# Performance work log

Hardware: AMD Instinct MI355X
Metric: run time of the kernel (lower is better)

## Reference

```python
import jax, jax.numpy as jnp
import numpy as np
from jax import lax

EPS = 1e-5
CLIP = 1.3  # Hardtanh(-1.3, 1.3)


def hardtanh(v):
    return jnp.clip(v, -CLIP, CLIP)


def binarize(v):
    # sign() forward with straight-through (identity) gradient, as in BCNN BinarizeF
    return v + lax.stop_gradient(jnp.sign(v) - v)


def bc_conv(x, w):
    # binarized conv: binarize both activations and weights, 3x3, stride 1, pad 1
    return lax.conv_general_dilated(
        binarize(x), binarize(w),
        window_strides=(1, 1), padding=((1, 1), (1, 1)),
        dimension_numbers=("NCHW", "OIHW", "NCHW"))


def batchnorm(v, gamma, beta):
    # batch statistics over (N, H, W), per-channel affine (DC_Bn4 variant)
    mean = jnp.mean(v, axis=(0, 2, 3), keepdims=True)
    var = jnp.var(v, axis=(0, 2, 3), keepdims=True)
    inv = lax.rsqrt(var + EPS)
    return (v - mean) * inv * gamma[None, :, None, None] + beta[None, :, None, None]


def setup_inputs() -> dict:
    key = jax.random.key(0)
    k_x, k_w1, k_w2 = jax.random.split(key, 3)
    C = 32
    x = jax.random.normal(k_x, (16, C, 224, 224), dtype=jnp.float32)
    w1 = jax.random.normal(k_w1, (C, C, 3, 3), dtype=jnp.float32) * 0.1
    w2 = jax.random.normal(k_w2, (C, C, 3, 3), dtype=jnp.float32) * 0.1
    g1 = jnp.ones((C,), jnp.float32); b1 = jnp.zeros((C,), jnp.float32)
    g2 = jnp.ones((C,), jnp.float32); b2 = jnp.zeros((C,), jnp.float32)
    return {"x": x, "w1": w1, "g1": g1, "b1": b1, "w2": w2, "g2": g2, "b2": b2}


def reference(x, w1, g1, b1, w2, g2, b2):
    y = batchnorm(bc_conv(hardtanh(x), w1), g1, b1)
    y = batchnorm(bc_conv(hardtanh(y), w2), g2, b2)
    return x + y
```

## Files before the change

kernel.cpp:

```cpp
#include <hip/hip_runtime.h>
#include <stdint.h>

#define NB 16
#define CC 32
#define HH 224
#define WW 224
#define HWP (HH*WW)
#define NHWP (NB*HWP)
#define PW 226
#define PSZ (PW*PW)

#define OFF_S1   0u
#define OFF_S2   3268864u
#define OFF_WP1  6537728u
#define OFF_WP2  6538880u
#define OFF_SQ1  6540032u
#define OFF_SQ2  6540288u
#define OFF_SUM1 6540544u
#define OFF_SUM2 6540672u

__global__ void __launch_bounds__(256) k_setup(const uint32_t* __restrict__ w1,
                                               const uint32_t* __restrict__ w2,
                                               char* __restrict__ ws) {
    int t = blockIdx.x * 256 + threadIdx.x;
    if (t < 576) {
        const uint32_t* w = (t < 288) ? w1 : w2;
        uint32_t* o = (uint32_t*)(ws + ((t < 288) ? OFF_WP1 : OFF_WP2));
        int idx = (t < 288) ? t : t - 288;
        int oc = idx / 9, k = idx - oc * 9;
        uint32_t word = 0;
        for (int i = 0; i < 32; ++i)
            word |= (w[(oc * 32 + i) * 9 + k] >> 31) << i;
        o[idx] = word;
    } else if (t < 768) {
        ((uint32_t*)(ws + OFF_SQ1))[t - 576] = 0u;
    } else if (t >= 1024 && t < 1024 + 28800) {
        int b = t - 1024;
        uint32_t* buf = (uint32_t*)(ws + ((b < 14400) ? OFF_S1 : OFF_S2));
        int bb = (b < 14400) ? b : b - 14400;
        int n = bb / 900;
        int e = bb - n * 900;
        int row, col;
        if (e < 226)      { row = 0;   col = e; }
        else if (e < 452) { row = 225; col = e - 226; }
        else { int k = e - 452; row = 1 + (k >> 1); col = (k & 1) ? 225 : 0; }
        buf[(size_t)n * PSZ + row * PW + col] = 0u;
    }
}

__global__ void __launch_bounds__(256) k_packx(const uint32_t* __restrict__ x,
                                               uint32_t* __restrict__ sp) {
    int t = blockIdx.x * 256 + threadIdx.x;
    int n = t / (HWP / 4);
    int rem4 = t - n * (HWP / 4);
    int px0 = rem4 * 4;
    int r = px0 / WW;
    int cw0 = px0 - r * WW;
    const uint32_t* xp = x + (size_t)n * CC * HWP + px0;
    uint32_t w0 = 0, w1 = 0, w2 = 0, w3 = 0;
    #pragma unroll
    for (int c = 0; c < 32; ++c) {
        uint4 v = *reinterpret_cast<const uint4*>(xp + (size_t)c * HWP);
        w0 |= (v.x >> 31) << c;
        w1 |= (v.y >> 31) << c;
        w2 |= (v.z >> 31) << c;
        w3 |= (v.w >> 31) << c;
    }
    uint32_t* op = sp + (size_t)n * PSZ + (r + 1) * PW + (cw0 + 1);
    op[0] = w0; op[1] = w1; op[2] = w2; op[3] = w3;
}

__device__ __forceinline__ void stage_lds(const uint32_t* __restrict__ wp,
                                          uint32_t (*Wl)[12], int (*Ctab)[32]) {
    for (int i = threadIdx.x; i < 288; i += 256) {
        int oc = i / 9, k = i - oc * 9;
        Wl[oc][k] = wp[i];
    }
    for (int i = threadIdx.x; i < 512; i += 256) {
        int ty = i >> 5, oc = i & 31;
        int s = 0;
        #pragma unroll
        for (int t = 0; t < 9; ++t) {
            int dh = t / 3 - 1, dw = t % 3 - 1;
            bool pad = ((ty & 1) && dh < 0) || ((ty & 2) && dh > 0) ||
                       ((ty & 4) && dw < 0) || ((ty & 8) && dw > 0);
            if (pad) s += 32 - 2 * __popc(wp[oc * 9 + t]);
        }
        Ctab[ty][oc] = s;
    }
}

__device__ __forceinline__ void decode_grp(int t, int& n, int& r, int& cw0) {
    n = t / 12544;
    int rem = t - n * 12544;
    r = rem / 56;
    cw0 = (rem - r * 56) * 4;
}

#define LOAD_TAPS18(base)                                                        \
    uint32_t u0 = (base)[-PW-1], u1 = (base)[-PW],   u2 = (base)[-PW+1],         \
             u3 = (base)[-PW+2], u4 = (base)[-PW+3], u5 = (base)[-PW+4];         \
    uint32_t m0 = (base)[-1],    m1 = (base)[0],     m2 = (base)[1],             \
             m3 = (base)[2],     m4 = (base)[3],     m5 = (base)[4];             \
    uint32_t l0 = (base)[PW-1],  l1 = (base)[PW],    l2 = (base)[PW+1],          \
             l3 = (base)[PW+2],  l4 = (base)[PW+3],  l5 = (base)[PW+4];

#define CONV4L(oc_)                                                              \
    int ocl = (oc_);                                                             \
    asm volatile("" : "+v"(ocl));                                                \
    const uint32_t* wr = &Wl[ocl][0];                                            \
    uint32_t w0 = wr[0], w1 = wr[1], w2 = wr[2], w3 = wr[3], w4 = wr[4],         \
             w5 = wr[5], w6 = wr[6], w7 = wr[7], w8 = wr[8];                     \
    int pc0 = __popc(u0^w0)+__popc(u1^w1)+__popc(u2^w2)                          \
            + __popc(m0^w3)+__popc(m1^w4)+__popc(m2^w5)                          \
            + __popc(l0^w6)+__popc(l1^w7)+__popc(l2^w8);                         \
    int pc1 = __popc(u1^w0)+__popc(u2^w1)+__popc(u3^w2)                          \
            + __popc(m1^w3)+__popc(m2^w4)+__popc(m3^w5)                          \
            + __popc(l1^w6)+__popc(l2^w7)+__popc(l3^w8);                         \
    int pc2 = __popc(u2^w0)+__popc(u3^w1)+__popc(u4^w2)                          \
            + __popc(m2^w3)+__popc(m3^w4)+__popc(m4^w5)                          \
            + __popc(l2^w6)+__popc(l3^w7)+__popc(l4^w8);                         \
    int pc3 = __popc(u3^w0)+__popc(u4^w1)+__popc(u5^w2)                          \
            + __popc(m3^w3)+__popc(m4^w4)+__popc(m5^w5)                          \
            + __popc(l3^w6)+__popc(l4^w7)+__popc(l5^w8);                         \
    int c0 = 288 - 2*pc0 - Ctab[ty0][ocl];                                       \
    int c1 = 288 - 2*pc1 - Ctab[rb][ocl];                                        \
    int c2 = 288 - 2*pc2 - Ctab[rb][ocl];                                        \
    int c3 = 288 - 2*pc3 - Ctab[ty3][ocl];

#define DECODE_BORDER()                                                          \
    int rb = (r == 0) ? 1 : (r == HH - 1) ? 2 : 0;                               \
    int ty0 = rb | ((cw0 == 0) ? 4 : 0);                                         \
    int ty3 = rb | ((cw0 == WW - 4) ? 8 : 0);

__global__ void __launch_bounds__(256) k_stats(const uint32_t* __restrict__ sp,
                                               const uint32_t* __restrict__ wp,
                                               int* __restrict__ g_sum,
                                               unsigned long long* __restrict__ g_sq) {
    __shared__ __align__(16) uint32_t Wl[32][12];
    __shared__ int Ctab[16][32];
    stage_lds(wp, Wl, Ctab);
    __syncthreads();

    int t = blockIdx.x * 256 + threadIdx.x;
    int n, r, cw0; decode_grp(t, n, r, cw0);
    const uint32_t* base = sp + (size_t)n * PSZ + (r + 1) * PW + (cw0 + 1);
    LOAD_TAPS18(base)
    DECODE_BORDER()

    int lane = threadIdx.x & 63;
    int lane31 = lane & 31;
    int myS = 0, myQ = 0;
    #pragma unroll
    for (int oc = 0; oc < 32; ++oc) {
        CONV4L(oc)
        int s = c0 + c1 + c2 + c3;
        int q = c0*c0 + c1*c1 + c2*c2 + c3*c3;
        #pragma unroll
        for (int d = 1; d <= 16; d <<= 1) {
            s += __shfl_xor(s, d, 64);
            q += __shfl_xor(q, d, 64);
        }
        if (lane31 == oc) { myS = s; myQ = q; }
    }
    myS += __shfl_xor(myS, 32, 64);
    myQ += __shfl_xor(myQ, 32, 64);

    __shared__ int ls[4][32], lq[4][32];
    int wid = threadIdx.x >> 6;
    if (lane < 32) { ls[wid][lane] = myS; lq[wid][lane] = myQ; }
    __syncthreads();
    if (threadIdx.x < 32) {
        int s = ls[0][threadIdx.x] + ls[1][threadIdx.x] + ls[2][threadIdx.x] + ls[3][threadIdx.x];
        int q = lq[0][threadIdx.x] + lq[1][threadIdx.x] + lq[2][threadIdx.x] + lq[3][threadIdx.x];
        atomicAdd(&g_sum[threadIdx.x], s);
        atomicAdd(&g_sq[threadIdx.x], (unsigned long long)(long long)q);
    }
}

__device__ __forceinline__ void build_affine(const int* __restrict__ g_sum,
                                             const unsigned long long* __restrict__ g_sq,
                                             const float* __restrict__ gamma,
                                             const float* __restrict__ beta,
                                             float* aL, float* dL) {
    if (threadIdx.x < 32) {
        int c = threadIdx.x;
        double M = (double)NHWP;
        double mean = (double)g_sum[c] / M;
        double ex2 = (double)(long long)g_sq[c] / M;
        double var = ex2 - mean * mean;
        double inv = 1.0 / sqrt(var + 1e-5);
        double aa = inv * (double)gamma[c];
        aL[c] = (float)aa;
        dL[c] = (float)((double)beta[c] - aa * mean);
    }
}

__global__ void __launch_bounds__(256) k_sign(const uint32_t* __restrict__ sp,
                                              const uint32_t* __restrict__ wp,
                                              const int* __restrict__ g_sum,
                                              const unsigned long long* __restrict__ g_sq,
                                              const float* __restrict__ gamma,
                                              const float* __restrict__ beta,
                                              uint32_t* __restrict__ op) {
    __shared__ __align__(16) uint32_t Wl[32][12];
    __shared__ int Ctab[16][32];
    __shared__ float aL[32], dL[32];
    stage_lds(wp, Wl, Ctab);
    build_affine(g_sum, g_sq, gamma, beta, aL, dL);
    __syncthreads();

    int t = blockIdx.x * 256 + threadIdx.x;
    int n, r, cw0; decode_grp(t, n, r, cw0);
    const uint32_t* base = sp + (size_t)n * PSZ + (r + 1) * PW + (cw0 + 1);
    LOAD_TAPS18(base)
    DECODE_BORDER()

    uint32_t wd0 = 0, wd1 = 0, wd2 = 0, wd3 = 0;
    #pragma unroll
    for (int oc = 0; oc < 32; ++oc) {
        CONV4L(oc)
        float a = aL[ocl], d = dL[ocl];
        wd0 |= (__float_as_uint(fmaf(a, (float)c0, d)) >> 31) << oc;
        wd1 |= (__float_as_uint(fmaf(a, (float)c1, d)) >> 31) << oc;
        wd2 |= (__float_as_uint(fmaf(a, (float)c2, d)) >> 31) << oc;
        wd3 |= (__float_as_uint(fmaf(a, (float)c3, d)) >> 31) << oc;
    }
    uint32_t* o = op + (size_t)n * PSZ + (r + 1) * PW + (cw0 + 1);
    o[0] = wd0; o[1] = wd1; o[2] = wd2; o[3] = wd3;
}

__global__ void __launch_bounds__(256) k_res(const uint32_t* __restrict__ sp,
                                             const uint32_t* __restrict__ wp,
                                             const int* __restrict__ g_sum,
                                             const unsigned long long* __restrict__ g_sq,
                                             const float* __restrict__ gamma,
                                             const float* __restrict__ beta,
                                             const float* __restrict__ x,
                                             float* __restrict__ out) {
    __shared__ __align__(16) uint32_t Wl[32][12];
    __shared__ int Ctab[16][32];
    __shared__ float aL[32], dL[32];
    stage_lds(wp, Wl, Ctab);
    build_affine(g_sum, g_sq, gamma, beta, aL, dL);
    __syncthreads();

    int t = blockIdx.x * 256 + threadIdx.x;
    int n, r, cw0; decode_grp(t, n, r, cw0);
    const uint32_t* base = sp + (size_t)n * PSZ + (r + 1) * PW + (cw0 + 1);
    LOAD_TAPS18(base)
    DECODE_BORDER()

    size_t pix = (size_t)n * CC * HWP + (size_t)r * WW + cw0;
    #pragma unroll
    for (int oc = 0; oc < 32; ++oc) {
        CONV4L(oc)
        float a = aL[ocl], d = dL[ocl];
        float4 xv = *reinterpret_cast<const float4*>(x + pix + (size_t)ocl * HWP);
        float4 ov;
        ov.x = xv.x + fmaf(a, (float)c0, d);
        ov.y = xv.y + fmaf(a, (float)c1, d);
        ov.z = xv.z + fmaf(a, (float)c2, d);
        ov.w = xv.w + fmaf(a, (float)c3, d);
        *reinterpret_cast<float4*>(out + pix + (size_t)ocl * HWP) = ov;
    }
}

extern "C" void kernel_launch(void* const* d_in, const int* in_sizes, int n_in,
                              void* d_out, int out_size, void* d_ws, size_t ws_size,
                              hipStream_t stream) {
    const float* x  = (const float*)d_in[0];
    const float* w1 = (const float*)d_in[1];
    const float* g1 = (const float*)d_in[2];
    const float* b1 = (const float*)d_in[3];
    const float* w2 = (const float*)d_in[4];
    const float* g2 = (const float*)d_in[5];
    const float* b2 = (const float*)d_in[6];
    float* out = (float*)d_out;

    char* ws = (char*)d_ws;
    uint32_t* s1  = (uint32_t*)(ws + OFF_S1);
    uint32_t* s2  = (uint32_t*)(ws + OFF_S2);
    uint32_t* wp1 = (uint32_t*)(ws + OFF_WP1);
    uint32_t* wp2 = (uint32_t*)(ws + OFF_WP2);
    unsigned long long* sq1 = (unsigned long long*)(ws + OFF_SQ1);
    unsigned long long* sq2 = (unsigned long long*)(ws + OFF_SQ2);
    int* sum1 = (int*)(ws + OFF_SUM1);
    int* sum2 = (int*)(ws + OFF_SUM2);

    k_setup<<<120, 256, 0, stream>>>((const uint32_t*)w1, (const uint32_t*)w2, ws);
    k_packx<<<784, 256, 0, stream>>>((const uint32_t*)x, s1);
    k_stats<<<784, 256, 0, stream>>>(s1, wp1, sum1, sq1);
    k_sign <<<784, 256, 0, stream>>>(s1, wp1, sum1, sq1, g1, b1, s2);
    k_stats<<<784, 256, 0, stream>>>(s2, wp2, sum2, sq2);
    k_res  <<<784, 256, 0, stream>>>(s2, wp2, sum2, sq2, g2, b2, x, out);
}
```

Before: 318.2 us.

## Replace XNOR-popcount binary conv with int8 MFMA in stats and sign kernels

```diff
diff --git a/kernel.cpp b/kernel.cpp
--- a/kernel.cpp
+++ b/kernel.cpp
@@ -15,9 +15,12 @@
 #define OFF_WP1  6537728u
 #define OFF_WP2  6538880u
 #define OFF_SQ1  6540032u
-#define OFF_SQ2  6540288u
-#define OFF_SUM1 6540544u
-#define OFF_SUM2 6540672u
+#define OFF_SQ2  6544128u
+#define OFF_SUM1 6548224u
+#define OFF_SUM2 6550272u
+
+typedef int v4i    __attribute__((ext_vector_type(4)));
+typedef int i32x16 __attribute__((ext_vector_type(16)));
 
 __global__ void __launch_bounds__(256) k_setup(const uint32_t* __restrict__ w1,
                                                const uint32_t* __restrict__ w2,
@@ -32,10 +35,10 @@
         for (int i = 0; i < 32; ++i)
             word |= (w[(oc * 32 + i) * 9 + k] >> 31) << i;
         o[idx] = word;
-    } else if (t < 768) {
+    } else if (t < 3648) {
         ((uint32_t*)(ws + OFF_SQ1))[t - 576] = 0u;
-    } else if (t >= 1024 && t < 1024 + 28800) {
-        int b = t - 1024;
+    } else if (t >= 4096 && t < 4096 + 28800) {
+        int b = t - 4096;
         uint32_t* buf = (uint32_t*)(ws + ((b < 14400) ? OFF_S1 : OFF_S2));
         int bb = (b < 14400) ? b : b - 14400;
         int n = bb / 900;
@@ -68,6 +71,143 @@
     }
     uint32_t* op = sp + (size_t)n * PSZ + (r + 1) * PW + (cw0 + 1);
     op[0] = w0; op[1] = w1; op[2] = w2; op[3] = w3;
+}
+
+#define ASTRIDE 48
+#define AROW (226*ASTRIDE)
+
+__device__ __forceinline__ uint32_t spread4(uint32_t nib) {
+    uint32_t s = (nib & 1u) | ((nib & 2u) << 7) | ((nib & 4u) << 14) | ((nib & 8u) << 21);
+    return 0x01010101u ^ (s * 0xFEu);
+}
+
+__device__ __forceinline__ i32x16 conv_mfma(const uint32_t* __restrict__ sp,
+                                            const uint32_t* __restrict__ wp,
+                                            int n, int r, char* At) {
+    for (int s = threadIdx.x; s < 3 * 226; s += 448) {
+        int dr = s / 226, cc = s - dr * 226;
+        int srow = r - 1 + dr, scol = cc - 1;
+        uint32_t d8[8];
+        if (srow < 0 || srow >= HH || scol < 0 || scol >= WW) {
+            #pragma unroll
+            for (int i = 0; i < 8; ++i) d8[i] = 0u;
+        } else {
+            uint32_t w = sp[(size_t)n * PSZ + (srow + 1) * PW + (scol + 1)];
+            #pragma unroll
+            for (int i = 0; i < 8; ++i) d8[i] = spread4((w >> (4 * i)) & 0xFu);
+        }
+        uint32_t* p = (uint32_t*)(At + s * ASTRIDE);
+        *(uint4*)(p)     = make_uint4(d8[0], d8[1], d8[2], d8[3]);
+        *(uint4*)(p + 4) = make_uint4(d8[4], d8[5], d8[6], d8[7]);
+    }
+
+    int l = threadIdx.x & 63;
+    int oc = l & 31, kb = (l >> 5) * 16;
+    v4i bf[9];
+    #pragma unroll
+    for (int t = 0; t < 9; ++t) {
+        uint32_t w = wp[oc * 9 + t];
+        uint32_t r0 = spread4((w >> (kb))      & 0xFu);
+        uint32_t r1 = spread4((w >> (kb + 4))  & 0xFu);
+        uint32_t r2 = spread4((w >> (kb + 8))  & 0xFu);
+        uint32_t r3 = spread4((w >> (kb + 12)) & 0xFu);
+        bf[t] = v4i{(int)r0, (int)r1, (int)r2, (int)r3};
+    }
+    __syncthreads();
+
+    int wavebase = (threadIdx.x >> 6) * 32;
+    int base = (wavebase + (l & 31)) * ASTRIDE + (l >> 5) * 16;
+
+    i32x16 acc = {0,0,0,0,0,0,0,0,0,0,0,0,0,0,0,0};
+    #pragma unroll
+    for (int dh = 0; dh < 3; ++dh) {
+        #pragma unroll
+        for (int dw = 0; dw < 3; ++dw) {
+            v4i a = *reinterpret_cast<const v4i*>(At + base + dh * AROW + dw * ASTRIDE);
+            acc = __builtin_amdgcn_mfma_i32_32x32x32_i8(a, bf[dh * 3 + dw], acc, 0, 0, 0);
+        }
+    }
+    return acc;
+}
+
+__global__ void __launch_bounds__(448) k_stats(const uint32_t* __restrict__ sp,
+                                               const uint32_t* __restrict__ wp,
+                                               int* __restrict__ g_sum,
+                                               unsigned long long* __restrict__ g_sq) {
+    __shared__ __align__(16) char At[3 * 226 * ASTRIDE];
+    __shared__ int ls[7][32], lq[7][32];
+
+    int n = blockIdx.x / HH, r = blockIdx.x - n * HH;
+    i32x16 acc = conv_mfma(sp, wp, n, r, At);
+
+    int l = threadIdx.x & 63;
+    int s = 0, q = 0;
+    #pragma unroll
+    for (int g = 0; g < 16; ++g) { int c = acc[g]; s += c; q += c * c; }
+    s += __shfl_xor(s, 32, 64);
+    q += __shfl_xor(q, 32, 64);
+    int wid = threadIdx.x >> 6;
+    if (l < 32) { ls[wid][l] = s; lq[wid][l] = q; }
+    __syncthreads();
+    if (threadIdx.x < 32) {
+        int S = 0, Q = 0;
+        #pragma unroll
+        for (int w = 0; w < 7; ++w) { S += ls[w][threadIdx.x]; Q += lq[w][threadIdx.x]; }
+        int bin = blockIdx.x & 15;
+        atomicAdd(&g_sum[bin * 32 + threadIdx.x], S);
+        atomicAdd(&g_sq[bin * 32 + threadIdx.x], (unsigned long long)(long long)Q);
+    }
+}
+
+__device__ __forceinline__ void build_affine16(const int* __restrict__ g_sum,
+                                               const unsigned long long* __restrict__ g_sq,
+                                               const float* __restrict__ gamma,
+                                               const float* __restrict__ beta,
+                                               float* aL, float* dL) {
+    if (threadIdx.x < 32) {
+        int c = threadIdx.x;
+        int Si = 0; unsigned long long Qu = 0;
+        #pragma unroll
+        for (int b = 0; b < 16; ++b) { Si += g_sum[b * 32 + c]; Qu += g_sq[b * 32 + c]; }
+        double M = (double)NHWP;
+        double mean = (double)Si / M;
+        double ex2 = (double)(long long)Qu / M;
+        double var = ex2 - mean * mean;
+        double inv = 1.0 / sqrt(var + 1e-5);
+        double aa = inv * (double)gamma[c];
+        aL[c] = (float)aa;
+        dL[c] = (float)((double)beta[c] - aa * mean);
+    }
+}
+
+__global__ void __launch_bounds__(448) k_sign(const uint32_t* __restrict__ sp,
+                                              const uint32_t* __restrict__ wp,
+                                              const int* __restrict__ g_sum,
+                                              const unsigned long long* __restrict__ g_sq,
+                                              const float* __restrict__ gamma,
+                                              const float* __restrict__ beta,
+                                              uint32_t* __restrict__ op) {
+    __shared__ __align__(16) char At[3 * 226 * ASTRIDE];
+    __shared__ float aL[32], dL[32];
+    build_affine16(g_sum, g_sq, gamma, beta, aL, dL);
+
+    int n = blockIdx.x / HH, r = blockIdx.x - n * HH;
+    i32x16 acc = conv_mfma(sp, wp, n, r, At);
+
+    int l = threadIdx.x & 63;
+    int wavebase = (threadIdx.x >> 6) * 32;
+    float a = aL[l & 31], d = dL[l & 31];
+    uint32_t* orow = op + (size_t)n * PSZ + (r + 1) * PW + 1 + wavebase;
+    #pragma unroll
+    for (int g = 0; g < 16; ++g) {
+        float y = fmaf(a, (float)acc[g], d);
+        unsigned long long b = __ballot((__float_as_uint(y) >> 31) != 0u);
+        if (l == 0) {
+            int pxr = (g & 3) + 8 * (g >> 2);
+            orow[pxr]     = (uint32_t)b;
+            orow[pxr + 4] = (uint32_t)(b >> 32);
+        }
+    }
 }
 
 __device__ __forceinline__ void stage_lds(const uint32_t* __restrict__ wp,
@@ -133,103 +273,6 @@
     int ty0 = rb | ((cw0 == 0) ? 4 : 0);                                         \
     int ty3 = rb | ((cw0 == WW - 4) ? 8 : 0);
 
-__global__ void __launch_bounds__(256) k_stats(const uint32_t* __restrict__ sp,
-                                               const uint32_t* __restrict__ wp,
-                                               int* __restrict__ g_sum,
-                                               unsigned long long* __restrict__ g_sq) {
-    __shared__ __align__(16) uint32_t Wl[32][12];
-    __shared__ int Ctab[16][32];
-    stage_lds(wp, Wl, Ctab);
-    __syncthreads();
-
-    int t = blockIdx.x * 256 + threadIdx.x;
-    int n, r, cw0; decode_grp(t, n, r, cw0);
-    const uint32_t* base = sp + (size_t)n * PSZ + (r + 1) * PW + (cw0 + 1);
-    LOAD_TAPS18(base)
-    DECODE_BORDER()
-
-    int lane = threadIdx.x & 63;
-    int lane31 = lane & 31;
-    int myS = 0, myQ = 0;
-    #pragma unroll
-    for (int oc = 0; oc < 32; ++oc) {
-        CONV4L(oc)
-        int s = c0 + c1 + c2 + c3;
-        int q = c0*c0 + c1*c1 + c2*c2 + c3*c3;
-        #pragma unroll
-        for (int d = 1; d <= 16; d <<= 1) {
-            s += __shfl_xor(s, d, 64);
-            q += __shfl_xor(q, d, 64);
-        }
-        if (lane31 == oc) { myS = s; myQ = q; }
-    }
-    myS += __shfl_xor(myS, 32, 64);
-    myQ += __shfl_xor(myQ, 32, 64);
-
-    __shared__ int ls[4][32], lq[4][32];
-    int wid = threadIdx.x >> 6;
-    if (lane < 32) { ls[wid][lane] = myS; lq[wid][lane] = myQ; }
-    __syncthreads();
-    if (threadIdx.x < 32) {
-        int s = ls[0][threadIdx.x] + ls[1][threadIdx.x] + ls[2][threadIdx.x] + ls[3][threadIdx.x];
-        int q = lq[0][threadIdx.x] + lq[1][threadIdx.x] + lq[2][threadIdx.x] + lq[3][threadIdx.x];
-        atomicAdd(&g_sum[threadIdx.x], s);
-        atomicAdd(&g_sq[threadIdx.x], (unsigned long long)(long long)q);
-    }
-}
-
-__device__ __forceinline__ void build_affine(const int* __restrict__ g_sum,
-                                             const unsigned long long* __restrict__ g_sq,
-                                             const float* __restrict__ gamma,
-                                             const float* __restrict__ beta,
-                                             float* aL, float* dL) {
-    if (threadIdx.x < 32) {
-        int c = threadIdx.x;
-        double M = (double)NHWP;
-        double mean = (double)g_sum[c] / M;
-        double ex2 = (double)(long long)g_sq[c] / M;
-        double var = ex2 - mean * mean;
-        double inv = 1.0 / sqrt(var + 1e-5);
-        double aa = inv * (double)gamma[c];
-        aL[c] = (float)aa;
-        dL[c] = (float)((double)beta[c] - aa * mean);
-    }
-}
-
-__global__ void __launch_bounds__(256) k_sign(const uint32_t* __restrict__ sp,
-                                              const uint32_t* __restrict__ wp,
-                                              const int* __restrict__ g_sum,
-                                              const unsigned long long* __restrict__ g_sq,
-                                              const float* __restrict__ gamma,
-                                              const float* __restrict__ beta,
-                                              uint32_t* __restrict__ op) {
-    __shared__ __align__(16) uint32_t Wl[32][12];
-    __shared__ int Ctab[16][32];
-    __shared__ float aL[32], dL[32];
-    stage_lds(wp, Wl, Ctab);
-    build_affine(g_sum, g_sq, gamma, beta, aL, dL);
-    __syncthreads();
-
-    int t = blockIdx.x * 256 + threadIdx.x;
-    int n, r, cw0; decode_grp(t, n, r, cw0);
-    const uint32_t* base = sp + (size_t)n * PSZ + (r + 1) * PW + (cw0 + 1);
-    LOAD_TAPS18(base)
-    DECODE_BORDER()
-
-    uint32_t wd0 = 0, wd1 = 0, wd2 = 0, wd3 = 0;
-    #pragma unroll
-    for (int oc = 0; oc < 32; ++oc) {
-        CONV4L(oc)
-        float a = aL[ocl], d = dL[ocl];
-        wd0 |= (__float_as_uint(fmaf(a, (float)c0, d)) >> 31) << oc;
-        wd1 |= (__float_as_uint(fmaf(a, (float)c1, d)) >> 31) << oc;
-        wd2 |= (__float_as_uint(fmaf(a, (float)c2, d)) >> 31) << oc;
-        wd3 |= (__float_as_uint(fmaf(a, (float)c3, d)) >> 31) << oc;
-    }
-    uint32_t* o = op + (size_t)n * PSZ + (r + 1) * PW + (cw0 + 1);
-    o[0] = wd0; o[1] = wd1; o[2] = wd2; o[3] = wd3;
-}
-
 __global__ void __launch_bounds__(256) k_res(const uint32_t* __restrict__ sp,
                                              const uint32_t* __restrict__ wp,
                                              const int* __restrict__ g_sum,
@@ -242,7 +285,7 @@
     __shared__ int Ctab[16][32];
     __shared__ float aL[32], dL[32];
     stage_lds(wp, Wl, Ctab);
-    build_affine(g_sum, g_sq, gamma, beta, aL, dL);
+    build_affine16(g_sum, g_sq, gamma, beta, aL, dL);
     __syncthreads();
 
     int t = blockIdx.x * 256 + threadIdx.x;
@@ -288,10 +331,10 @@
     int* sum1 = (int*)(ws + OFF_SUM1);
     int* sum2 = (int*)(ws + OFF_SUM2);
 
-    k_setup<<<120, 256, 0, stream>>>((const uint32_t*)w1, (const uint32_t*)w2, ws);
+    k_setup<<<132, 256, 0, stream>>>((const uint32_t*)w1, (const uint32_t*)w2, ws);
     k_packx<<<784, 256, 0, stream>>>((const uint32_t*)x, s1);
-    k_stats<<<784, 256, 0, stream>>>(s1, wp1, sum1, sq1);
-    k_sign <<<784, 256, 0, stream>>>(s1, wp1, sum1, sq1, g1, b1, s2);
-    k_stats<<<784, 256, 0, stream>>>(s2, wp2, sum2, sq2);
+    k_stats<<<3584, 448, 0, stream>>>(s1, wp1, sum1, sq1);
+    k_sign <<<3584, 448, 0, stream>>>(s1, wp1, sum1, sq1, g1, b1, s2);
+    k_stats<<<3584, 448, 0, stream>>>(s2, wp2, sum2, sq2);
     k_res  <<<784, 256, 0, stream>>>(s2, wp2, sum2, sq2, g2, b2, x, out);
 }
```

Measured after the change: 320.1 us. About the same (+0.6%).
